# Optimization experiments

Hardware: AMD Instinct MI355X
Metric: run time of the kernel (lower is better)

Reference implementation:

```python
import jax, jax.numpy as jnp
import numpy as np

NUM_EMBEDDINGS = 1024
LATENT_SIZE = 256
N = 131072


def setup_inputs() -> dict:
    key = jax.random.key(0)
    k1, k2 = jax.random.split(key)
    inputs = jax.random.normal(k1, (N, LATENT_SIZE), dtype=jnp.float32)
    embed = jax.random.normal(k2, (LATENT_SIZE, NUM_EMBEDDINGS), dtype=jnp.float32)
    return {"inputs": inputs, "embed": embed}


def reference(inputs, embed):
    # Squared Euclidean distances: [N, K]
    dist = (
        jnp.sum(inputs * inputs, axis=1, keepdims=True)
        - 2.0 * (inputs @ embed)
        + jnp.sum(embed * embed, axis=0, keepdims=True)
    )
    embed_ind = jnp.argmin(dist, axis=1)  # [N]
    embed_onehot = jax.nn.one_hot(embed_ind, NUM_EMBEDDINGS, dtype=inputs.dtype)  # [N, K]
    # Gather codebook vectors: embedding lookup into embed.T -> [N, D]
    quantize = embed.T[embed_ind]
    # Commitment-style loss (eval path: no EMA buffer updates)
    loss = jnp.mean((jax.lax.stop_gradient(quantize) - inputs) ** 2)
    # Straight-through estimator
    quantize = inputs + jax.lax.stop_gradient(quantize - inputs)
    avg_probs = jnp.mean(embed_onehot, axis=0)  # [K]
    perplexity = jnp.exp(-jnp.sum(avg_probs * jnp.log(avg_probs + 1e-10)))
    return quantize, loss, perplexity, embed_ind
```

## Files before the change

kernel.cpp:

```cpp
#include <hip/hip_runtime.h>
#include <math.h>

#define M_ROWS 131072
#define D_DIM 256
#define NCODES 1024
#define QELEMS (M_ROWS * D_DIM)

typedef __attribute__((ext_vector_type(8))) short short8v;
typedef __attribute__((ext_vector_type(4))) float f32x4;
typedef unsigned short ushort_t;

#define WS_EMBEDT 0u
#define WS_B1     1048576u
#define WS_B2     1572864u
#define WS_ENORM  2097152u
#define WS_PART   2101248u
#define WS_IDX2   18878464u
#define WS_COUNTS 19927040u
#define WS_LOSSP  19931136u
#define WS_XHI    19963904u
#define WS_XLO    87072768u
#define WS_FAST_TOTAL 154181632u

typedef unsigned int u32_g __attribute__((address_space(1)));
typedef unsigned int u32_l __attribute__((address_space(3)));
__device__ inline void gll16(const void* g, void* l) {
  __builtin_amdgcn_global_load_lds((const u32_g*)g, (u32_l*)l, 16, 0, 0);
}

__device__ inline unsigned pack2(float x, float y) {
  return __builtin_amdgcn_perm(__float_as_uint(y), __float_as_uint(x), 0x07060302u);
}
__device__ inline float rem1(float x) {
  return x - __uint_as_float(__float_as_uint(x) & 0xFFFF0000u);
}
__device__ inline void split8(float4 a, float4 b, uint4* hi, uint4* lo) {
  *hi = make_uint4(pack2(a.x, a.y), pack2(a.z, a.w), pack2(b.x, b.y), pack2(b.z, b.w));
  *lo = make_uint4(pack2(rem1(a.x), rem1(a.y)), pack2(rem1(a.z), rem1(a.w)),
                   pack2(rem1(b.x), rem1(b.y)), pack2(rem1(b.z), rem1(b.w)));
}

__device__ inline void merge2(float& b0, int& i0, float& b1, int& i1,
                              float o0, int oi0, float o1, int oi1) {
  if (o0 < b0 || (o0 == b0 && oi0 < i0)) {
    if (b0 < o1 || (b0 == o1 && i0 < oi1)) { b1 = b0; i1 = i0; }
    else { b1 = o1; i1 = oi1; }
    b0 = o0; i0 = oi0;
  } else {
    if (o0 < b1 || (o0 == b1 && oi0 < i1)) { b1 = o0; i1 = oi0; }
  }
}

__global__ __launch_bounds__(256) void k_prep(const float* __restrict__ embed,
                                              float* __restrict__ embedT,
                                              ushort_t* __restrict__ b1,
                                              ushort_t* __restrict__ b2,
                                              float* __restrict__ enorm, int fast) {
  int c = blockIdx.x, t = threadIdx.x;
  float v = embed[t * NCODES + c];
  embedT[c * D_DIM + t] = v;
  unsigned bits = __float_as_uint(v);
  ushort_t hi = (ushort_t)(bits >> 16);
  ushort_t lo = (ushort_t)(__float_as_uint(rem1(v)) >> 16);
  if (fast) {
    int ct = c >> 7, cl = c & 127, kc = t >> 5, u = (t >> 3) & 3, j = t & 7;
    size_t off = (size_t)(ct * 8 + kc) * 4096 + cl * 32 + ((u ^ (cl & 3)) << 3) + j;
    b1[off] = hi; b2[off] = lo;
  } else {
    b1[c * D_DIM + t] = hi;
    b2[c * D_DIM + t] = lo;
  }
  float s = v * v;
  for (int off = 32; off > 0; off >>= 1) s += __shfl_down(s, off, 64);
  __shared__ float red[4];
  if ((t & 63) == 0) red[t >> 6] = s;
  __syncthreads();
  if (t == 0) enorm[c] = red[0] + red[1] + red[2] + red[3];
}

__global__ __launch_bounds__(256) void k_asplit(const float* __restrict__ x,
                                                ushort_t* __restrict__ xhi,
                                                ushort_t* __restrict__ xlo) {
  int rt = blockIdx.x, t = threadIdx.x;
  int sr = t >> 1;
  int kh = (t & 1) << 4;
  int s3 = sr & 3;
  const float* row = x + ((size_t)(rt << 7) + sr) * D_DIM + kh;
  size_t tb = (size_t)rt * 32768;
#pragma unroll
  for (int kc = 0; kc < 8; ++kc) {
    float4 v0 = *(const float4*)(row + kc * 32 + 0);
    float4 v1 = *(const float4*)(row + kc * 32 + 4);
    float4 v2 = *(const float4*)(row + kc * 32 + 8);
    float4 v3 = *(const float4*)(row + kc * 32 + 12);
    uint4 h0, l0, h1, l1;
    split8(v0, v1, &h0, &l0);
    split8(v2, v3, &h1, &l1);
    int u0 = kh >> 3;
    size_t base = tb + (size_t)kc * 4096 + sr * 32;
    *(uint4*)&xhi[base + ((u0 ^ s3) << 3)] = h0;
    *(uint4*)&xhi[base + (((u0 + 1) ^ s3) << 3)] = h1;
    *(uint4*)&xlo[base + ((u0 ^ s3) << 3)] = l0;
    *(uint4*)&xlo[base + (((u0 + 1) ^ s3) << 3)] = l1;
  }
}

__device__ inline void dist_epilogue(f32x4 (&acc)[4][4], const float* __restrict__ enorm,
                                     float4* __restrict__ partials, float4 (*sRed)[128],
                                     int t, int wr, int wc, int lm, int quad,
                                     int rowBase, int colBase, int ct) {
  float enC[4]; int cidx[4];
#pragma unroll
  for (int j = 0; j < 4; ++j) {
    cidx[j] = colBase + (wc << 6) + (j << 4) + lm;
    enC[j] = enorm[cidx[j]];
  }
#pragma unroll
  for (int ti = 0; ti < 4; ++ti) {
#pragma unroll
    for (int reg = 0; reg < 4; ++reg) {
      float b0 = 3.0e38f, b1 = 3.0e38f;
      int i0 = 0x7fffffff, i1 = 0x7fffffff;
#pragma unroll
      for (int j = 0; j < 4; ++j) {
        float v = fmaf(-2.f, acc[ti][j][reg], enC[j]);
        int c = cidx[j];
        if (v < b0 || (v == b0 && c < i0)) { b1 = b0; i1 = i0; b0 = v; i0 = c; }
        else if (v < b1 || (v == b1 && c < i1)) { b1 = v; i1 = c; }
      }
      for (int m = 1; m < 16; m <<= 1) {
        float o0 = __shfl_xor(b0, m, 64); int oi0 = __shfl_xor(i0, m, 64);
        float o1 = __shfl_xor(b1, m, 64); int oi1 = __shfl_xor(i1, m, 64);
        merge2(b0, i0, b1, i1, o0, oi0, o1, oi1);
      }
      if (lm == 0) {
        int rloc = (wr << 6) + (ti << 4) + (quad << 2) + reg;
        sRed[wc][rloc] = make_float4(b0, (float)i0, b1, (float)i1);
      }
    }
  }
  __syncthreads();
  if (t < 128) {
    float4 p = sRed[0][t];
    float b0 = p.x; int i0 = (int)p.y; float b1 = p.z; int i1 = (int)p.w;
    float4 q = sRed[1][t];
    merge2(b0, i0, b1, i1, q.x, (int)q.y, q.z, (int)q.w);
    partials[(size_t)ct * M_ROWS + rowBase + t] = make_float4(b0, (float)i0, b1, (float)i1);
  }
}

__global__ __launch_bounds__(256, 3) void k_dist_fast(const ushort_t* __restrict__ xhi,
                                                      const ushort_t* __restrict__ xlo,
                                                      const ushort_t* __restrict__ bhi,
                                                      const ushort_t* __restrict__ blo,
                                                      const float* __restrict__ enorm,
                                                      float4* __restrict__ partials) {
  __shared__ ushort_t sAhi[4096], sAlo[4096], sBhi[4096], sBlo[4096];
  __shared__ float4 sRed[2][128];

  int bx = blockIdx.x;
  int xcd = bx & 7, slot = bx >> 3;
  int rt = (xcd << 7) | (slot >> 3);
  int ct = slot & 7;
  int rowBase = rt << 7, colBase = ct << 7;
  int t = threadIdx.x;
  int w = t >> 6, lane = t & 63;
  int wr = w >> 1, wc = w & 1;
  int lm = lane & 15, quad = lane >> 4;

  f32x4 acc[4][4];
#pragma unroll
  for (int i = 0; i < 4; ++i)
#pragma unroll
    for (int j = 0; j < 4; ++j) acc[i][j] = (f32x4){0.f, 0.f, 0.f, 0.f};

  int aoff[4], boff[4];
#pragma unroll
  for (int ti = 0; ti < 4; ++ti) {
    int r = (wr << 6) + (ti << 4) + lm;
    aoff[ti] = r * 32 + ((quad ^ (r & 3)) << 3);
    int n = (wc << 6) + (ti << 4) + lm;
    boff[ti] = n * 32 + ((quad ^ (n & 3)) << 3);
  }

  int c0 = w << 1;
  int src0 = c0 * 512 + lane * 8;
  const ushort_t* gA = xhi + (size_t)rt * 32768;
  const ushort_t* gAl = xlo + (size_t)rt * 32768;
  const ushort_t* gB = bhi + (size_t)ct * 32768;
  const ushort_t* gBl = blo + (size_t)ct * 32768;

  for (int kc = 0; kc < 8; ++kc) {
    int src = kc * 4096 + src0;
    gll16(gA + src, &sAhi[c0 * 512]);
    gll16(gA + src + 512, &sAhi[(c0 + 1) * 512]);
    gll16(gAl + src, &sAlo[c0 * 512]);
    gll16(gAl + src + 512, &sAlo[(c0 + 1) * 512]);
    gll16(gB + src, &sBhi[c0 * 512]);
    gll16(gB + src + 512, &sBhi[(c0 + 1) * 512]);
    gll16(gBl + src, &sBlo[c0 * 512]);
    gll16(gBl + src + 512, &sBlo[(c0 + 1) * 512]);
    __syncthreads();

    short8v ahi[4], bhi_f[4];
#pragma unroll
    for (int i = 0; i < 4; ++i) {
      ahi[i] = *(const short8v*)&sAhi[aoff[i]];
      bhi_f[i] = *(const short8v*)&sBhi[boff[i]];
    }
#pragma unroll
    for (int i = 0; i < 4; ++i)
#pragma unroll
      for (int j = 0; j < 4; ++j)
        acc[i][j] = __builtin_amdgcn_mfma_f32_16x16x32_bf16(ahi[i], bhi_f[j], acc[i][j], 0, 0, 0);
    short8v blo_f[4];
#pragma unroll
    for (int i = 0; i < 4; ++i) blo_f[i] = *(const short8v*)&sBlo[boff[i]];
#pragma unroll
    for (int i = 0; i < 4; ++i)
#pragma unroll
      for (int j = 0; j < 4; ++j)
        acc[i][j] = __builtin_amdgcn_mfma_f32_16x16x32_bf16(ahi[i], blo_f[j], acc[i][j], 0, 0, 0);
    short8v alo[4];
#pragma unroll
    for (int i = 0; i < 4; ++i) alo[i] = *(const short8v*)&sAlo[aoff[i]];
#pragma unroll
    for (int i = 0; i < 4; ++i)
#pragma unroll
      for (int j = 0; j < 4; ++j)
        acc[i][j] = __builtin_amdgcn_mfma_f32_16x16x32_bf16(alo[i], bhi_f[j], acc[i][j], 0, 0, 0);
    __syncthreads();
  }

  dist_epilogue(acc, enorm, partials, sRed, t, wr, wc, lm, quad, rowBase, colBase, ct);
}

__global__ __launch_bounds__(256, 3) void k_dist_slow(const float* __restrict__ A,
                                                      const ushort_t* __restrict__ ehiT,
                                                      const ushort_t* __restrict__ eloT,
                                                      const float* __restrict__ enorm,
                                                      float4* __restrict__ partials) {
  __shared__ ushort_t sAhi[4096], sAlo[4096], sBhi[4096], sBlo[4096];
  __shared__ float4 sRed[2][128];

  int bx = blockIdx.x;
  int ct = bx & 7, rt = bx >> 3;
  int rowBase = rt << 7, colBase = ct << 7;
  int t = threadIdx.x;
  int w = t >> 6, lane = t & 63;
  int wr = w >> 1, wc = w & 1;
  int lm = lane & 15, quad = lane >> 4;
  int sr = t >> 1;
  int skh = (t & 1) << 4;

  f32x4 acc[4][4];
#pragma unroll
  for (int i = 0; i < 4; ++i)
#pragma unroll
    for (int j = 0; j < 4; ++j) acc[i][j] = (f32x4){0.f, 0.f, 0.f, 0.f};

  int aoff[4], boff[4];
#pragma unroll
  for (int ti = 0; ti < 4; ++ti) {
    int r = (wr << 6) + (ti << 4) + lm;
    aoff[ti] = r * 32 + ((quad ^ (r & 3)) << 3);
    int n = (wc << 6) + (ti << 4) + lm;
    boff[ti] = n * 32 + ((quad ^ (n & 3)) << 3);
  }

  const float* Arow = A + (size_t)(rowBase + sr) * D_DIM + skh;
  const ushort_t* Bhirow = ehiT + (size_t)(colBase + sr) * D_DIM + skh;
  const ushort_t* Blorow = eloT + (size_t)(colBase + sr) * D_DIM + skh;

  for (int kc = 0; kc < D_DIM; kc += 32) {
#pragma unroll
    for (int u = 0; u < 4; ++u) {
      float4 v = *(const float4*)(Arow + kc + (u << 2));
      int koff = skh + (u << 2);
      int dst = sr * 32 + (((koff >> 3) ^ (sr & 3)) << 3) + (koff & 7);
      *(uint2*)&sAhi[dst] = make_uint2(pack2(v.x, v.y), pack2(v.z, v.w));
      *(uint2*)&sAlo[dst] = make_uint2(pack2(rem1(v.x), rem1(v.y)), pack2(rem1(v.z), rem1(v.w)));
    }
#pragma unroll
    for (int h = 0; h < 2; ++h) {
      int koff = skh + (h << 3);
      int dst = sr * 32 + (((koff >> 3) ^ (sr & 3)) << 3);
      *(uint4*)&sBhi[dst] = *(const uint4*)(Bhirow + kc + (h << 3));
      *(uint4*)&sBlo[dst] = *(const uint4*)(Blorow + kc + (h << 3));
    }
    __syncthreads();

    short8v ahi[4], bhi_f[4], blo_f[4], alo[4];
#pragma unroll
    for (int i = 0; i < 4; ++i) {
      ahi[i] = *(const short8v*)&sAhi[aoff[i]];
      bhi_f[i] = *(const short8v*)&sBhi[boff[i]];
      blo_f[i] = *(const short8v*)&sBlo[boff[i]];
      alo[i] = *(const short8v*)&sAlo[aoff[i]];
    }
#pragma unroll
    for (int i = 0; i < 4; ++i)
#pragma unroll
      for (int j = 0; j < 4; ++j)
        acc[i][j] = __builtin_amdgcn_mfma_f32_16x16x32_bf16(ahi[i], bhi_f[j], acc[i][j], 0, 0, 0);
#pragma unroll
    for (int i = 0; i < 4; ++i)
#pragma unroll
      for (int j = 0; j < 4; ++j)
        acc[i][j] = __builtin_amdgcn_mfma_f32_16x16x32_bf16(ahi[i], blo_f[j], acc[i][j], 0, 0, 0);
#pragma unroll
    for (int i = 0; i < 4; ++i)
#pragma unroll
      for (int j = 0; j < 4; ++j)
        acc[i][j] = __builtin_amdgcn_mfma_f32_16x16x32_bf16(alo[i], bhi_f[j], acc[i][j], 0, 0, 0);
    __syncthreads();
  }

  dist_epilogue(acc, enorm, partials, sRed, t, wr, wc, lm, quad, rowBase, colBase, ct);
}

__global__ __launch_bounds__(256) void k_argmin(const float4* __restrict__ partials,
                                                int2* __restrict__ idx2) {
  int row = blockIdx.x * 256 + threadIdx.x;
  float b0 = 3.0e38f, b1 = 3.0e38f;
  int i0 = 0x7fffffff, i1 = 0x7fffffff;
#pragma unroll
  for (int tp = 0; tp < 8; ++tp) {
    float4 p = partials[(size_t)tp * M_ROWS + row];
    merge2(b0, i0, b1, i1, p.x, (int)p.y, p.z, (int)p.w);
  }
  idx2[row] = make_int2(i0, i1);
}

__global__ __launch_bounds__(256) void k_quant(const float* __restrict__ x,
                                               const float* __restrict__ embedT,
                                               const int2* __restrict__ idx2,
                                               float* __restrict__ outq,
                                               float* __restrict__ out_ind,
                                               int* __restrict__ counts,
                                               float* __restrict__ lossPart) {
  int b = blockIdx.x, t = threadIdx.x;
  int rl = t >> 6, lane = t & 63;
  float lsum = 0.f;
  __shared__ float red[4];
#pragma unroll
  for (int ri = 0; ri < 4; ++ri) {
    int row = b * 16 + ri * 4 + rl;
    int2 cc = idx2[row];
    float4 xv = *(const float4*)(x + (size_t)row * D_DIM + (lane << 2));
    float4 q0 = *(const float4*)(embedT + (size_t)cc.x * D_DIM + (lane << 2));
    float4 q1 = *(const float4*)(embedT + (size_t)cc.y * D_DIM + (lane << 2));
    float a0 = q0.x - xv.x, a1 = q0.y - xv.y, a2 = q0.z - xv.z, a3 = q0.w - xv.w;
    float c0 = q1.x - xv.x, c1 = q1.y - xv.y, c2 = q1.z - xv.z, c3 = q1.w - xv.w;
    float d0 = fmaf(a0, a0, fmaf(a1, a1, fmaf(a2, a2, a3 * a3)));
    float d1 = fmaf(c0, c0, fmaf(c1, c1, fmaf(c2, c2, c3 * c3)));
    for (int m = 1; m < 64; m <<= 1) {
      d0 += __shfl_xor(d0, m, 64);
      d1 += __shfl_xor(d1, m, 64);
    }
    bool sel = (d1 < d0) || (d1 == d0 && cc.y < cc.x);
    int widx = sel ? cc.y : cc.x;
    float4 qv;
    qv.x = sel ? q1.x : q0.x; qv.y = sel ? q1.y : q0.y;
    qv.z = sel ? q1.z : q0.z; qv.w = sel ? q1.w : q0.w;
    float4 o = make_float4(xv.x + (qv.x - xv.x), xv.y + (qv.y - xv.y),
                           xv.z + (qv.z - xv.z), xv.w + (qv.w - xv.w));
    *(float4*)(outq + (size_t)row * D_DIM + (lane << 2)) = o;
    lsum += sel ? d1 : d0;
    if (lane == 0) {
      out_ind[row] = (float)widx;
      atomicAdd(&counts[widx], 1);
    }
  }
  if (lane == 0) red[rl] = lsum;
  __syncthreads();
  if (t == 0) lossPart[b] = red[0] + red[1] + red[2] + red[3];
}

__global__ __launch_bounds__(1024) void k_final(const int* __restrict__ counts,
                                                const float* __restrict__ lossPart,
                                                float* __restrict__ out_scalars) {
  int t = threadIdx.x;
  double ls = 0.0;
#pragma unroll
  for (int u = 0; u < 8; ++u) ls += (double)lossPart[t * 8 + u];
  float p = (float)counts[t] * (1.0f / (float)M_ROWS);
  float ent = p * logf(p + 1e-10f);
  double lred = ls;
  float ered = ent;
  for (int off = 32; off > 0; off >>= 1) {
    lred += __shfl_down(lred, off, 64);
    ered += __shfl_down(ered, off, 64);
  }
  __shared__ double lsh[16];
  __shared__ float esh[16];
  int w = t >> 6;
  if ((t & 63) == 0) { lsh[w] = lred; esh[w] = ered; }
  __syncthreads();
  if (t == 0) {
    double L = 0.0;
    float E = 0.f;
    for (int i = 0; i < 16; ++i) { L += lsh[i]; E += esh[i]; }
    out_scalars[0] = (float)(L / (double)QELEMS);
    out_scalars[1] = expf(-E);
  }
}

extern "C" void kernel_launch(void* const* d_in, const int* in_sizes, int n_in,
                              void* d_out, int out_size, void* d_ws, size_t ws_size,
                              hipStream_t stream) {
  const float* inputs = (const float*)d_in[0];
  const float* embed = (const float*)d_in[1];
  float* out = (float*)d_out;
  char* ws = (char*)d_ws;
  float* embedT = (float*)(ws + WS_EMBEDT);
  ushort_t* b1 = (ushort_t*)(ws + WS_B1);
  ushort_t* b2 = (ushort_t*)(ws + WS_B2);
  float* enorm = (float*)(ws + WS_ENORM);
  float4* partials = (float4*)(ws + WS_PART);
  int2* idx2 = (int2*)(ws + WS_IDX2);
  int* counts = (int*)(ws + WS_COUNTS);
  float* lossPart = (float*)(ws + WS_LOSSP);
  ushort_t* xhi = (ushort_t*)(ws + WS_XHI);
  ushort_t* xlo = (ushort_t*)(ws + WS_XLO);

  int fast = (ws_size >= (size_t)WS_FAST_TOTAL) ? 1 : 0;

  hipMemsetAsync(counts, 0, NCODES * sizeof(int), stream);
  k_prep<<<NCODES, 256, 0, stream>>>(embed, embedT, b1, b2, enorm, fast);
  if (fast) {
    k_asplit<<<M_ROWS / 128, 256, 0, stream>>>(inputs, xhi, xlo);
    k_dist_fast<<<8192, 256, 0, stream>>>(xhi, xlo, b1, b2, enorm, partials);
  } else {
    k_dist_slow<<<8192, 256, 0, stream>>>(inputs, b1, b2, enorm, partials);
  }
  k_argmin<<<M_ROWS / 256, 256, 0, stream>>>(partials, idx2);
  k_quant<<<8192, 256, 0, stream>>>(inputs, embedT, idx2, out, out + QELEMS + 2,
                                    counts, lossPart);
  k_final<<<1, 1024, 0, stream>>>(counts, lossPart, out + QELEMS);
}
```

Measured before the change: 924.3 us.

## Load MFMA operands directly from fragment-ordered global layout, dropping LDS staging

Reorders the split bf16 hi/lo input and codebook buffers into per-wave MFMA fragment order so the fast distance kernel loads operands straight from global memory into registers. This removes the LDS staging and both block barriers per k-chunk. In exchange, A and B tiles are no longer shared across waves through LDS, so global/L2 traffic roughly doubles and register pressure rises. The slow fallback path also gets a different LDS swizzle to reduce bank conflicts.

```diff
diff --git a/kernel.cpp b/kernel.cpp
--- a/kernel.cpp
+++ b/kernel.cpp
@@ -21,12 +21,6 @@
 #define WS_XHI    19963904u
 #define WS_XLO    87072768u
 #define WS_FAST_TOTAL 154181632u
-
-typedef unsigned int u32_g __attribute__((address_space(1)));
-typedef unsigned int u32_l __attribute__((address_space(3)));
-__device__ inline void gll16(const void* g, void* l) {
-  __builtin_amdgcn_global_load_lds((const u32_g*)g, (u32_l*)l, 16, 0, 0);
-}
 
 __device__ inline unsigned pack2(float x, float y) {
   return __builtin_amdgcn_perm(__float_as_uint(y), __float_as_uint(x), 0x07060302u);
@@ -63,8 +57,10 @@
   ushort_t hi = (ushort_t)(bits >> 16);
   ushort_t lo = (ushort_t)(__float_as_uint(rem1(v)) >> 16);
   if (fast) {
-    int ct = c >> 7, cl = c & 127, kc = t >> 5, u = (t >> 3) & 3, j = t & 7;
-    size_t off = (size_t)(ct * 8 + kc) * 4096 + cl * 32 + ((u ^ (cl & 3)) << 3) + j;
+    int cg = c >> 6, ti = (c >> 4) & 3, lm = c & 15;
+    int kc = t >> 5, quad = (t >> 3) & 3, j = t & 7;
+    int lane = quad * 16 + lm;
+    size_t off = ((size_t)((cg * 8 + kc) * 4 + ti) * 64 + lane) * 8 + j;
     b1[off] = hi; b2[off] = lo;
   } else {
     b1[c * D_DIM + t] = hi;
@@ -81,27 +77,20 @@
 __global__ __launch_bounds__(256) void k_asplit(const float* __restrict__ x,
                                                 ushort_t* __restrict__ xhi,
                                                 ushort_t* __restrict__ xlo) {
-  int rt = blockIdx.x, t = threadIdx.x;
-  int sr = t >> 1;
-  int kh = (t & 1) << 4;
-  int s3 = sr & 3;
-  const float* row = x + ((size_t)(rt << 7) + sr) * D_DIM + kh;
-  size_t tb = (size_t)rt * 32768;
+  int g = blockIdx.x, t = threadIdx.x;
+  int ti = t >> 6, lane = t & 63;
+  int quad = lane >> 4, lm = lane & 15;
+  int row = g * 64 + ti * 16 + lm;
+  const float* src = x + (size_t)row * D_DIM + quad * 8;
+  size_t dst = (size_t)g * 16384 + ti * 512 + (size_t)lane * 8;
 #pragma unroll
   for (int kc = 0; kc < 8; ++kc) {
-    float4 v0 = *(const float4*)(row + kc * 32 + 0);
-    float4 v1 = *(const float4*)(row + kc * 32 + 4);
-    float4 v2 = *(const float4*)(row + kc * 32 + 8);
-    float4 v3 = *(const float4*)(row + kc * 32 + 12);
-    uint4 h0, l0, h1, l1;
-    split8(v0, v1, &h0, &l0);
-    split8(v2, v3, &h1, &l1);
-    int u0 = kh >> 3;
-    size_t base = tb + (size_t)kc * 4096 + sr * 32;
-    *(uint4*)&xhi[base + ((u0 ^ s3) << 3)] = h0;
-    *(uint4*)&xhi[base + (((u0 + 1) ^ s3) << 3)] = h1;
-    *(uint4*)&xlo[base + ((u0 ^ s3) << 3)] = l0;
-    *(uint4*)&xlo[base + (((u0 + 1) ^ s3) << 3)] = l1;
+    float4 v0 = *(const float4*)(src + kc * 32);
+    float4 v1 = *(const float4*)(src + kc * 32 + 4);
+    uint4 h, l;
+    split8(v0, v1, &h, &l);
+    *(uint4*)&xhi[dst + (size_t)kc * 2048] = h;
+    *(uint4*)&xlo[dst + (size_t)kc * 2048] = l;
   }
 }
 
@@ -155,7 +144,6 @@
                                                       const ushort_t* __restrict__ blo,
                                                       const float* __restrict__ enorm,
                                                       float4* __restrict__ partials) {
-  __shared__ ushort_t sAhi[4096], sAlo[4096], sBhi[4096], sBlo[4096];
   __shared__ float4 sRed[2][128];
 
   int bx = blockIdx.x;
@@ -168,68 +156,46 @@
   int wr = w >> 1, wc = w & 1;
   int lm = lane & 15, quad = lane >> 4;
 
+  int g = rt * 2 + wr;
+  int cg = ct * 2 + wc;
+
+  const ushort_t* pAh = xhi + (size_t)g * 16384 + (size_t)lane * 8;
+  const ushort_t* pAl = xlo + (size_t)g * 16384 + (size_t)lane * 8;
+  const ushort_t* pBh = bhi + (size_t)cg * 16384 + (size_t)lane * 8;
+  const ushort_t* pBl = blo + (size_t)cg * 16384 + (size_t)lane * 8;
+
   f32x4 acc[4][4];
 #pragma unroll
   for (int i = 0; i < 4; ++i)
 #pragma unroll
     for (int j = 0; j < 4; ++j) acc[i][j] = (f32x4){0.f, 0.f, 0.f, 0.f};
 
-  int aoff[4], boff[4];
-#pragma unroll
-  for (int ti = 0; ti < 4; ++ti) {
-    int r = (wr << 6) + (ti << 4) + lm;
-    aoff[ti] = r * 32 + ((quad ^ (r & 3)) << 3);
-    int n = (wc << 6) + (ti << 4) + lm;
-    boff[ti] = n * 32 + ((quad ^ (n & 3)) << 3);
-  }
-
-  int c0 = w << 1;
-  int src0 = c0 * 512 + lane * 8;
-  const ushort_t* gA = xhi + (size_t)rt * 32768;
-  const ushort_t* gAl = xlo + (size_t)rt * 32768;
-  const ushort_t* gB = bhi + (size_t)ct * 32768;
-  const ushort_t* gBl = blo + (size_t)ct * 32768;
-
+#pragma unroll
   for (int kc = 0; kc < 8; ++kc) {
-    int src = kc * 4096 + src0;
-    gll16(gA + src, &sAhi[c0 * 512]);
-    gll16(gA + src + 512, &sAhi[(c0 + 1) * 512]);
-    gll16(gAl + src, &sAlo[c0 * 512]);
-    gll16(gAl + src + 512, &sAlo[(c0 + 1) * 512]);
-    gll16(gB + src, &sBhi[c0 * 512]);
-    gll16(gB + src + 512, &sBhi[(c0 + 1) * 512]);
-    gll16(gBl + src, &sBlo[c0 * 512]);
-    gll16(gBl + src + 512, &sBlo[(c0 + 1) * 512]);
-    __syncthreads();
-
-    short8v ahi[4], bhi_f[4];
+    int base = kc * 2048;
+    short8v ahi_f[4], alo_f[4], bhi_f[4], blo_f[4];
 #pragma unroll
     for (int i = 0; i < 4; ++i) {
-      ahi[i] = *(const short8v*)&sAhi[aoff[i]];
-      bhi_f[i] = *(const short8v*)&sBhi[boff[i]];
-    }
-#pragma unroll
-    for (int i = 0; i < 4; ++i)
-#pragma unroll
-      for (int j = 0; j < 4; ++j)
-        acc[i][j] = __builtin_amdgcn_mfma_f32_16x16x32_bf16(ahi[i], bhi_f[j], acc[i][j], 0, 0, 0);
-    short8v blo_f[4];
-#pragma unroll
-    for (int i = 0; i < 4; ++i) blo_f[i] = *(const short8v*)&sBlo[boff[i]];
-#pragma unroll
-    for (int i = 0; i < 4; ++i)
-#pragma unroll
-      for (int j = 0; j < 4; ++j)
-        acc[i][j] = __builtin_amdgcn_mfma_f32_16x16x32_bf16(ahi[i], blo_f[j], acc[i][j], 0, 0, 0);
-    short8v alo[4];
-#pragma unroll
-    for (int i = 0; i < 4; ++i) alo[i] = *(const short8v*)&sAlo[aoff[i]];
-#pragma unroll
-    for (int i = 0; i < 4; ++i)
-#pragma unroll
-      for (int j = 0; j < 4; ++j)
-        acc[i][j] = __builtin_amdgcn_mfma_f32_16x16x32_bf16(alo[i], bhi_f[j], acc[i][j], 0, 0, 0);
-    __syncthreads();
+      ahi_f[i] = *(const short8v*)(pAh + base + i * 512);
+      bhi_f[i] = *(const short8v*)(pBh + base + i * 512);
+      blo_f[i] = *(const short8v*)(pBl + base + i * 512);
+      alo_f[i] = *(const short8v*)(pAl + base + i * 512);
+    }
+#pragma unroll
+    for (int i = 0; i < 4; ++i)
+#pragma unroll
+      for (int j = 0; j < 4; ++j)
+        acc[i][j] = __builtin_amdgcn_mfma_f32_16x16x32_bf16(ahi_f[i], bhi_f[j], acc[i][j], 0, 0, 0);
+#pragma unroll
+    for (int i = 0; i < 4; ++i)
+#pragma unroll
+      for (int j = 0; j < 4; ++j)
+        acc[i][j] = __builtin_amdgcn_mfma_f32_16x16x32_bf16(ahi_f[i], blo_f[j], acc[i][j], 0, 0, 0);
+#pragma unroll
+    for (int i = 0; i < 4; ++i)
+#pragma unroll
+      for (int j = 0; j < 4; ++j)
+        acc[i][j] = __builtin_amdgcn_mfma_f32_16x16x32_bf16(alo_f[i], bhi_f[j], acc[i][j], 0, 0, 0);
   }
 
   dist_epilogue(acc, enorm, partials, sRed, t, wr, wc, lm, quad, rowBase, colBase, ct);
@@ -263,28 +229,29 @@
 #pragma unroll
   for (int ti = 0; ti < 4; ++ti) {
     int r = (wr << 6) + (ti << 4) + lm;
-    aoff[ti] = r * 32 + ((quad ^ (r & 3)) << 3);
+    aoff[ti] = r * 32 + ((quad ^ ((r >> 1) & 3)) << 3);
     int n = (wc << 6) + (ti << 4) + lm;
-    boff[ti] = n * 32 + ((quad ^ (n & 3)) << 3);
+    boff[ti] = n * 32 + ((quad ^ ((n >> 1) & 3)) << 3);
   }
 
   const float* Arow = A + (size_t)(rowBase + sr) * D_DIM + skh;
   const ushort_t* Bhirow = ehiT + (size_t)(colBase + sr) * D_DIM + skh;
   const ushort_t* Blorow = eloT + (size_t)(colBase + sr) * D_DIM + skh;
+  int ssw = (sr >> 1) & 3;
 
   for (int kc = 0; kc < D_DIM; kc += 32) {
 #pragma unroll
     for (int u = 0; u < 4; ++u) {
       float4 v = *(const float4*)(Arow + kc + (u << 2));
       int koff = skh + (u << 2);
-      int dst = sr * 32 + (((koff >> 3) ^ (sr & 3)) << 3) + (koff & 7);
+      int dst = sr * 32 + (((koff >> 3) ^ ssw) << 3) + (koff & 7);
       *(uint2*)&sAhi[dst] = make_uint2(pack2(v.x, v.y), pack2(v.z, v.w));
       *(uint2*)&sAlo[dst] = make_uint2(pack2(rem1(v.x), rem1(v.y)), pack2(rem1(v.z), rem1(v.w)));
     }
 #pragma unroll
     for (int h = 0; h < 2; ++h) {
       int koff = skh + (h << 3);
-      int dst = sr * 32 + (((koff >> 3) ^ (sr & 3)) << 3);
+      int dst = sr * 32 + (((koff >> 3) ^ ssw) << 3);
       *(uint4*)&sBhi[dst] = *(const uint4*)(Bhirow + kc + (h << 3));
       *(uint4*)&sBlo[dst] = *(const uint4*)(Blorow + kc + (h << 3));
     }
@@ -429,7 +396,7 @@
   hipMemsetAsync(counts, 0, NCODES * sizeof(int), stream);
   k_prep<<<NCODES, 256, 0, stream>>>(embed, embedT, b1, b2, enorm, fast);
   if (fast) {
-    k_asplit<<<M_ROWS / 128, 256, 0, stream>>>(inputs, xhi, xlo);
+    k_asplit<<<M_ROWS / 64, 256, 0, stream>>>(inputs, xhi, xlo);
     k_dist_fast<<<8192, 256, 0, stream>>>(xhi, xlo, b1, b2, enorm, partials);
   } else {
     k_dist_slow<<<8192, 256, 0, stream>>>(inputs, b1, b2, enorm, partials);
```

Measured after the change: 1.002 ms. 1.08x slower.
